# Kernel tuning notes

Hardware: AMD Instinct MI355X
Metric: run time of the kernel (lower is better)

The kernel has to match this reference:

```python
import jax, jax.numpy as jnp
import numpy as np

D_MODEL = 1024
NUM_HEADS = 16
ROPE_THETA = 10000.0


def setup_inputs() -> dict:
    key = jax.random.key(0)
    ks = jax.random.split(key, 5)
    B, S, D = 4, 2048, D_MODEL
    std = (2.0 / (D * D)) ** 0.5
    return {
        "x": jax.random.normal(ks[0], (B, S, D), dtype=jnp.float32),
        "Wq": jax.random.normal(ks[1], (D, D), dtype=jnp.float32) * std,
        "Wk": jax.random.normal(ks[2], (D, D), dtype=jnp.float32) * std,
        "Wv": jax.random.normal(ks[3], (D, D), dtype=jnp.float32) * std,
        "Wo": jax.random.normal(ks[4], (D, D), dtype=jnp.float32) * std,
    }


def _apply_rope(t, sin, cos):
    # t: [B, H, S, d_k]; sin/cos: [S, d_k//2] (broadcast over B, H)
    e = t[..., 0::2]
    o = t[..., 1::2]
    rot = jnp.stack((e * cos - o * sin, e * sin + o * cos), axis=-1)
    return rot.reshape(t.shape)  # interleave back to d_k


def reference(x, Wq, Wk, Wv, Wo):
    B, S, D = x.shape
    H = NUM_HEADS
    dk = D // H

    def proj(W):
        y = jnp.einsum('bsd,ed->bse', x, W)  # Linear: weight is [out, in]
        return y.reshape(B, S, H, dk).transpose(0, 2, 1, 3)  # [B,H,S,dk]

    q, k, v = proj(Wq), proj(Wk), proj(Wv)

    # RoPE cache (token_positions = arange(S))
    half = dk // 2
    inv_freq = 1.0 / (ROPE_THETA ** (jnp.arange(half, dtype=jnp.float32) * 2.0 / dk))
    angles = jnp.arange(S, dtype=jnp.float32)[:, None] * inv_freq[None, :]  # [S, half]
    sin, cos = jnp.sin(angles), jnp.cos(angles)
    q = _apply_rope(q, sin, cos)
    k = _apply_rope(k, sin, cos)

    # scaled dot-product attention with causal mask
    scores = jnp.einsum('bhqd,bhkd->bhqk', q, k) / jnp.sqrt(jnp.float32(dk))
    causal = jnp.tril(jnp.ones((S, S), dtype=bool))
    scores = jnp.where(causal, scores, jnp.finfo(scores.dtype).min)
    p = jax.nn.softmax(scores, axis=-1)
    out = jnp.einsum('bhqk,bhkd->bhqd', p, v)  # [B,H,S,dk]

    out = out.transpose(0, 2, 1, 3).reshape(B, S, D)
    return jnp.einsum('bsd,ed->bse', out, Wo)
```

## Files before the change

kernel.cpp:

```cpp
#include <hip/hip_runtime.h>

typedef unsigned short u16;
typedef unsigned int   u32;

typedef short    short8 __attribute__((ext_vector_type(8)));
typedef __bf16   bf16x8 __attribute__((ext_vector_type(8)));
typedef _Float16 half8  __attribute__((ext_vector_type(8)));
typedef float    f32x4  __attribute__((ext_vector_type(4)));

#define S_LEN   2048
#define DM      1024
#define NHEAD   16
#define DK      64
#define BH_TOT  64
#define M_TOK   8192
#define KDIM    1024

__device__ __forceinline__ u16 f2bf(float f) {
    u32 u = __builtin_bit_cast(u32, f);
    u += 0x7FFFu + ((u >> 16) & 1u);
    return (u16)(u >> 16);
}
__device__ __forceinline__ float bf2f(u16 h) {
    u32 u = ((u32)h) << 16;
    return __builtin_bit_cast(float, u);
}
__device__ __forceinline__ f32x4 mfma_bf16(short8 a, short8 b, f32x4 c) {
    return __builtin_amdgcn_mfma_f32_16x16x32_bf16(
        __builtin_bit_cast(bf16x8, a), __builtin_bit_cast(bf16x8, b), c, 0, 0, 0);
}
__device__ __forceinline__ f32x4 mfma_f16(half8 a, half8 b, f32x4 c) {
    return __builtin_amdgcn_mfma_f32_16x16x32_f16(a, b, c, 0, 0, 0);
}
__device__ __forceinline__ u32 pk_f16(float a, float b) {
    return __builtin_bit_cast(u32, __builtin_amdgcn_cvt_pkrtz(a, b));
}
__device__ __forceinline__ void gl_lds16(const void* g, void* l) {
    __builtin_amdgcn_global_load_lds(
        (const __attribute__((address_space(1))) u32*)g,
        (__attribute__((address_space(3))) u32*)l, 16, 0, 0);
}
__device__ __forceinline__ void bar_raw() { asm volatile("s_barrier" ::: "memory"); }
__device__ __forceinline__ void wait_vm4() { asm volatile("s_waitcnt vmcnt(4)" ::: "memory"); }
__device__ __forceinline__ void wait_vm0() { asm volatile("s_waitcnt vmcnt(0)" ::: "memory"); }

__device__ __forceinline__ int perm_inv(int rc) {
    const int nt = rc >> 4, mid = (rc >> 2) & 3, r = rc & 3;
    return 32 * (nt >> 1) + 8 * mid + 4 * (nt & 1) + r;
}

__global__ void cvt_bf16_v4(const float4* __restrict__ in, uint2* __restrict__ out, int n4) {
    int i = blockIdx.x * 256 + threadIdx.x;
    if (i >= n4) return;
    float4 f = in[i];
    uint2 o;
    o.x = (u32)f2bf(f.x) | ((u32)f2bf(f.y) << 16);
    o.y = (u32)f2bf(f.z) | ((u32)f2bf(f.w) << 16);
    out[i] = o;
}

__global__ void rope_qk(u16* __restrict__ Qb, u16* __restrict__ Kb) {
    int idx = blockIdx.x * 256 + threadIdx.x;
    const int PER = BH_TOT * S_LEN * 32;
    u16* T = (idx < PER) ? Qb : Kb;
    int i2 = (idx < PER) ? idx : idx - PER;
    int i  = i2 & 31;
    int s  = (i2 >> 5) & 2047;
    int bh = i2 >> 16;
    u32* p = (u32*)T + (size_t)(bh * S_LEN + s) * 32 + i;
    u32 v = *p;
    float e = bf2f((u16)(v & 0xFFFF));
    float o = bf2f((u16)(v >> 16));
    float inv = expf(-(float)i * 0.287823136624255f);
    float ang = (float)s * inv;
    float sn = sinf(ang), cs = cosf(ang);
    float e2 = e * cs - o * sn;
    float o2 = e * sn + o * cs;
    *p = (u32)f2bf(e2) | ((u32)f2bf(o2) << 16);
}

template <int MODE>
__global__ __launch_bounds__(256)
void gemm_nt(const u16* __restrict__ A, const u16* __restrict__ Bw,
             u16* __restrict__ oQ, u16* __restrict__ oK, u16* __restrict__ oVt,
             float* __restrict__ oF) {
    __shared__ u16 As[128 * 32];
    __shared__ u16 Bs[128 * 32];
    const int tid  = threadIdx.x;
    const int wave = tid >> 6, lane = tid & 63;
    const int quad = lane >> 4, l15 = lane & 15;
    const int wr = wave >> 1, wc = wave & 1;
    const int mbase = blockIdx.y * 128;
    const int nbase = blockIdx.x * 128;

    f32x4 acc[4][4];
#pragma unroll
    for (int i = 0; i < 4; i++)
#pragma unroll
        for (int j = 0; j < 4; j++) acc[i][j] = (f32x4)0.0f;

    const int c0 = wave * 2, c1 = wave * 2 + 1;
    const int srow0 = c0 * 16 + (lane >> 2);
    const int srow1 = c1 * 16 + (lane >> 2);
    const int scolb = (lane & 3) * 16;

    for (int kk = 0; kk < KDIM; kk += 32) {
        gl_lds16((const char*)(A  + (size_t)(mbase + srow0) * KDIM + kk) + scolb,
                 (char*)As + c0 * 1024 + lane * 16);
        gl_lds16((const char*)(A  + (size_t)(mbase + srow1) * KDIM + kk) + scolb,
                 (char*)As + c1 * 1024 + lane * 16);
        gl_lds16((const char*)(Bw + (size_t)(nbase + srow0) * KDIM + kk) + scolb,
                 (char*)Bs + c0 * 1024 + lane * 16);
        gl_lds16((const char*)(Bw + (size_t)(nbase + srow1) * KDIM + kk) + scolb,
                 (char*)Bs + c1 * 1024 + lane * 16);
        __syncthreads();

        short8 af[4], bf[4];
#pragma unroll
        for (int mt = 0; mt < 4; mt++)
            af[mt] = *(const short8*)&As[(wr * 64 + mt * 16 + l15) * 32 + quad * 8];
#pragma unroll
        for (int nt = 0; nt < 4; nt++)
            bf[nt] = *(const short8*)&Bs[(wc * 64 + nt * 16 + l15) * 32 + quad * 8];
#pragma unroll
        for (int mt = 0; mt < 4; mt++)
#pragma unroll
            for (int nt = 0; nt < 4; nt++)
                acc[mt][nt] = mfma_bf16(af[mt], bf[nt], acc[mt][nt]);
        __syncthreads();
    }

#pragma unroll
    for (int mt = 0; mt < 4; mt++) {
#pragma unroll
        for (int nt = 0; nt < 4; nt++) {
            const int n  = nbase + wc * 64 + nt * 16 + l15;
            const int mb = mbase + wr * 64 + mt * 16 + quad * 4;
            f32x4 v = acc[mt][nt];
            if (MODE == 0) {
                const int proj = n >> 10;
                const int e = n & 1023;
                const int h = e >> 6, d = e & 63;
                if (proj == 2) {
                    const int b = mb >> 11, s = mb & 2047;
                    const int bh = b * NHEAD + h;
                    uint2 pk;
                    pk.x = pk_f16(v[0], v[1]);
                    pk.y = pk_f16(v[2], v[3]);
                    *(uint2*)&oVt[((size_t)bh * DK + d) * S_LEN + s] = pk;
                } else {
                    u16* dst = (proj == 0) ? oQ : oK;
#pragma unroll
                    for (int r = 0; r < 4; r++) {
                        const int m = mb + r;
                        const int b = m >> 11, s = m & 2047;
                        const int bh = b * NHEAD + h;
                        dst[((size_t)bh * S_LEN + s) * DK + d] = f2bf(v[r]);
                    }
                }
            } else {
#pragma unroll
                for (int r = 0; r < 4; r++)
                    oF[(size_t)(mb + r) * DM + n] = v[r];
            }
        }
    }
}

__global__ __launch_bounds__(256)
void flash_attn(const u16* __restrict__ Q, const u16* __restrict__ K,
                const u16* __restrict__ Vt, u16* __restrict__ Oc) {
    __shared__ u16 Ks[2][64 * 64];
    __shared__ u16 Vs[2][64 * 64];
    const int qt = 31 - (int)blockIdx.y;
    const int bh = blockIdx.x;
    const int tid  = threadIdx.x;
    const int wave = tid >> 6, lane = tid & 63;
    const int quad = lane >> 4, l15 = lane & 15;
    const int x7 = l15 & 7;
    const size_t headQK = (size_t)bh * S_LEN * DK;
    const size_t headVt = (size_t)bh * DK * S_LEN;
    const int b = bh >> 4, h = bh & 15;
    const float SCL = 0.18033688011112042f;

    half8 ones;
#pragma unroll
    for (int j = 0; j < 8; j++) ones[j] = (_Float16)1.0f;

    const int rwl  = lane >> 3;
    const int scol = (lane & 7) ^ rwl;
    const int rc0 = wave * 16 + rwl, rc1 = rc0 + 8;
    const u16* gK0 = K  + headQK + (size_t)perm_inv(rc0) * DK + scol * 8;
    const u16* gK1 = K  + headQK + (size_t)perm_inv(rc1) * DK + scol * 8;
    const u16* gV0 = Vt + headVt + (size_t)rc0 * S_LEN + scol * 8;
    const u16* gV1 = Vt + headVt + (size_t)rc1 * S_LEN + scol * 8;
    const int ldsOff = wave * 2048 + lane * 16;
    const int koff0 = (quad ^ x7) * 8;
    const int koff1 = ((4 + quad) ^ x7) * 8;

    const int qrow = qt * 64 + wave * 16 + l15;
    const short8 qf0 = *(const short8*)&Q[headQK + (size_t)qrow * DK + quad * 8];
    const short8 qf1 = *(const short8*)&Q[headQK + (size_t)qrow * DK + 32 + quad * 8];

    float m_st = -__builtin_inff();
    f32x4 lacc = (f32x4)0.0f;
    f32x4 oacc[4];
#pragma unroll
    for (int n = 0; n < 4; n++) oacc[n] = (f32x4)0.0f;

    gl_lds16(gK0, (char*)Ks[0] + ldsOff);
    gl_lds16(gK1, (char*)Ks[0] + ldsOff + 1024);
    gl_lds16(gV0, (char*)Vs[0] + ldsOff);
    gl_lds16(gV1, (char*)Vs[0] + ldsOff + 1024);

    for (int kt = 0; kt <= qt; kt++) {
        const int cur = kt & 1, nxt = cur ^ 1;
        bar_raw();
        {
            const int ktn = (kt < qt) ? kt + 1 : qt;
            gl_lds16(gK0 + (size_t)ktn * 64 * DK, (char*)Ks[nxt] + ldsOff);
            gl_lds16(gK1 + (size_t)ktn * 64 * DK, (char*)Ks[nxt] + ldsOff + 1024);
            gl_lds16(gV0 + ktn * 64,              (char*)Vs[nxt] + ldsOff);
            gl_lds16(gV1 + ktn * 64,              (char*)Vs[nxt] + ldsOff + 1024);
        }
        wait_vm4();
        bar_raw();

        f32x4 sc[4];
#pragma unroll
        for (int nt = 0; nt < 4; nt++) {
            const int rb = (nt * 16 + l15) * 64;
            short8 kf0 = *(const short8*)&Ks[cur][rb + koff0];
            short8 kf1 = *(const short8*)&Ks[cur][rb + koff1];
            f32x4 z = (f32x4)0.0f;
            z = mfma_bf16(kf0, qf0, z);
            z = mfma_bf16(kf1, qf1, z);
#pragma unroll
            for (int r = 0; r < 4; r++) z[r] *= SCL;
            sc[nt] = z;
        }
        if (kt == qt) {
            const int qloc = wave * 16 + l15;
#pragma unroll
            for (int nt = 0; nt < 4; nt++) {
                const int kb = 32 * (nt >> 1) + 8 * quad + 4 * (nt & 1);
#pragma unroll
                for (int r = 0; r < 4; r++)
                    if (kb + r > qloc) sc[nt][r] = -__builtin_inff();
            }
        }
        float mx0 = fmaxf(fmaxf(sc[0][0], sc[0][1]), fmaxf(sc[0][2], sc[0][3]));
        float mx1 = fmaxf(fmaxf(sc[1][0], sc[1][1]), fmaxf(sc[1][2], sc[1][3]));
        float mx2 = fmaxf(fmaxf(sc[2][0], sc[2][1]), fmaxf(sc[2][2], sc[2][3]));
        float mx3 = fmaxf(fmaxf(sc[3][0], sc[3][1]), fmaxf(sc[3][2], sc[3][3]));
        float mx = fmaxf(fmaxf(mx0, mx1), fmaxf(mx2, mx3));
        mx = fmaxf(mx, __shfl_xor(mx, 16));
        mx = fmaxf(mx, __shfl_xor(mx, 32));
        const float mn = fmaxf(m_st, mx);
        const float alpha = __builtin_amdgcn_exp2f(m_st - mn);
        m_st = mn;
#pragma unroll
        for (int nt = 0; nt < 4; nt++)
#pragma unroll
            for (int r = 0; r < 4; r++)
                sc[nt][r] = __builtin_amdgcn_exp2f(sc[nt][r] - m_st);
        u32 pw[8];
        pw[0] = pk_f16(sc[0][0], sc[0][1]); pw[1] = pk_f16(sc[0][2], sc[0][3]);
        pw[2] = pk_f16(sc[1][0], sc[1][1]); pw[3] = pk_f16(sc[1][2], sc[1][3]);
        pw[4] = pk_f16(sc[2][0], sc[2][1]); pw[5] = pk_f16(sc[2][2], sc[2][3]);
        pw[6] = pk_f16(sc[3][0], sc[3][1]); pw[7] = pk_f16(sc[3][2], sc[3][3]);
        half8 pf0 = __builtin_bit_cast(half8, *(uint4*)&pw[0]);
        half8 pf1 = __builtin_bit_cast(half8, *(uint4*)&pw[4]);
        float alr[4];
#pragma unroll
        for (int r = 0; r < 4; r++) alr[r] = __shfl(alpha, quad * 20 + r);
#pragma unroll
        for (int n = 0; n < 4; n++)
#pragma unroll
            for (int r = 0; r < 4; r++) oacc[n][r] *= alr[r];
#pragma unroll
        for (int r = 0; r < 4; r++) lacc[r] *= alr[r];
#pragma unroll
        for (int c = 0; c < 2; c++) {
            const half8 pf = c ? pf1 : pf0;
            lacc = mfma_f16(pf, ones, lacc);
            const int voff = ((c * 4 + quad) ^ x7) * 8;
#pragma unroll
            for (int nt2 = 0; nt2 < 4; nt2++) {
                half8 vf = __builtin_bit_cast(half8,
                    *(const short8*)&Vs[cur][(nt2 * 16 + l15) * 64 + voff]);
                oacc[nt2] = mfma_f16(pf, vf, oacc[nt2]);
            }
        }
    }
    wait_vm0();

#pragma unroll
    for (int r = 0; r < 4; r++) {
        const float inv = 1.0f / lacc[r];
        const int s = qt * 64 + wave * 16 + quad * 4 + r;
#pragma unroll
        for (int nt2 = 0; nt2 < 4; nt2++)
            Oc[((size_t)(b * S_LEN + s)) * DM + h * 64 + nt2 * 16 + l15] =
                f2bf(oacc[nt2][r] * inv);
    }
}

#define OFF_XBF  ((size_t)0)
#define OFF_WCAT ((size_t)8388608)
#define OFF_WO   ((size_t)11534336)
#define OFF_QB   ((size_t)12582912)
#define OFF_KB   ((size_t)20971520)
#define OFF_VT   ((size_t)29360128)

extern "C" void kernel_launch(void* const* d_in, const int* in_sizes, int n_in,
                              void* d_out, int out_size, void* d_ws, size_t ws_size,
                              hipStream_t stream) {
    const float* x  = (const float*)d_in[0];
    const float* Wq = (const float*)d_in[1];
    const float* Wk = (const float*)d_in[2];
    const float* Wv = (const float*)d_in[3];
    const float* Wo = (const float*)d_in[4];
    u16* ws  = (u16*)d_ws;
    u16* XBF = ws + OFF_XBF;
    u16* WCA = ws + OFF_WCAT;
    u16* WOB = ws + OFF_WO;
    u16* QB  = ws + OFF_QB;
    u16* KB  = ws + OFF_KB;
    u16* VT  = ws + OFF_VT;
    u16* AT  = XBF;

    cvt_bf16_v4<<<8192, 256, 0, stream>>>((const float4*)x,  (uint2*)XBF, 2097152);
    cvt_bf16_v4<<<1024, 256, 0, stream>>>((const float4*)Wq, (uint2*)(WCA),            262144);
    cvt_bf16_v4<<<1024, 256, 0, stream>>>((const float4*)Wk, (uint2*)(WCA + 1048576),  262144);
    cvt_bf16_v4<<<1024, 256, 0, stream>>>((const float4*)Wv, (uint2*)(WCA + 2097152),  262144);
    cvt_bf16_v4<<<1024, 256, 0, stream>>>((const float4*)Wo, (uint2*)WOB, 262144);

    gemm_nt<0><<<dim3(24, 64), 256, 0, stream>>>(XBF, WCA, QB, KB, VT, nullptr);
    rope_qk<<<32768, 256, 0, stream>>>(QB, KB);
    flash_attn<<<dim3(64, 32), 256, 0, stream>>>(QB, KB, VT, AT);
    gemm_nt<1><<<dim3(8, 64), 256, 0, stream>>>(AT, WOB, nullptr, nullptr, nullptr,
                                                (float*)d_out);
}
```

Baseline: 291.3 us.

## Double-buffer GEMM LDS tiles with async prefetch and XOR swizzle

Converts the projection GEMM main loop to double-buffered LDS so the next K-tile's direct global-to-LDS loads are issued before computing on the current tile, with explicit vmcnt waits and raw barriers. It also XOR-swizzles the 16-byte column chunks in LDS to cut bank conflicts on the MFMA fragment reads. The aim is to hide global load latency behind the MFMAs, at the cost of double the shared memory per block, which may lower occupancy. The last iteration issues a redundant reload of the same tile.

New measurement: 296.3 us. Within noise of the previous version (+1.7%).

```diff
diff --git a/kernel.cpp b/kernel.cpp
--- a/kernel.cpp
+++ b/kernel.cpp
@@ -84,8 +84,8 @@
 void gemm_nt(const u16* __restrict__ A, const u16* __restrict__ Bw,
              u16* __restrict__ oQ, u16* __restrict__ oK, u16* __restrict__ oVt,
              float* __restrict__ oF) {
-    __shared__ u16 As[128 * 32];
-    __shared__ u16 Bs[128 * 32];
+    __shared__ u16 As[2][128 * 32];
+    __shared__ u16 Bs[2][128 * 32];
     const int tid  = threadIdx.x;
     const int wave = tid >> 6, lane = tid & 63;
     const int quad = lane >> 4, l15 = lane & 15;
@@ -99,36 +99,49 @@
 #pragma unroll
         for (int j = 0; j < 4; j++) acc[i][j] = (f32x4)0.0f;
 
-    const int c0 = wave * 2, c1 = wave * 2 + 1;
-    const int srow0 = c0 * 16 + (lane >> 2);
-    const int srow1 = c1 * 16 + (lane >> 2);
-    const int scolb = (lane & 3) * 16;
-
-    for (int kk = 0; kk < KDIM; kk += 32) {
-        gl_lds16((const char*)(A  + (size_t)(mbase + srow0) * KDIM + kk) + scolb,
-                 (char*)As + c0 * 1024 + lane * 16);
-        gl_lds16((const char*)(A  + (size_t)(mbase + srow1) * KDIM + kk) + scolb,
-                 (char*)As + c1 * 1024 + lane * 16);
-        gl_lds16((const char*)(Bw + (size_t)(nbase + srow0) * KDIM + kk) + scolb,
-                 (char*)Bs + c0 * 1024 + lane * 16);
-        gl_lds16((const char*)(Bw + (size_t)(nbase + srow1) * KDIM + kk) + scolb,
-                 (char*)Bs + c1 * 1024 + lane * 16);
-        __syncthreads();
+    const int srow0 = wave * 32 + (lane >> 2);
+    const int srow1 = srow0 + 16;
+    const int scolb = ((lane & 3) ^ ((lane >> 3) & 3)) * 16;
+    const int ldsOff = wave * 2048 + lane * 16;
+    const u16* gA0 = A  + (size_t)(mbase + srow0) * KDIM;
+    const u16* gA1 = A  + (size_t)(mbase + srow1) * KDIM;
+    const u16* gB0 = Bw + (size_t)(nbase + srow0) * KDIM;
+    const u16* gB1 = Bw + (size_t)(nbase + srow1) * KDIM;
+    const int koffq = (quad ^ ((l15 >> 1) & 3)) * 8;
+
+    gl_lds16((const char*)gA0 + scolb, (char*)As[0] + ldsOff);
+    gl_lds16((const char*)gA1 + scolb, (char*)As[0] + ldsOff + 1024);
+    gl_lds16((const char*)gB0 + scolb, (char*)Bs[0] + ldsOff);
+    gl_lds16((const char*)gB1 + scolb, (char*)Bs[0] + ldsOff + 1024);
+
+    const int KT = KDIM / 32;
+    for (int kt = 0; kt < KT; kt++) {
+        const int cur = kt & 1, nxt = cur ^ 1;
+        bar_raw();
+        {
+            const int kkn = (kt + 1 < KT) ? (kt + 1) * 32 : kt * 32;
+            gl_lds16((const char*)(gA0 + kkn) + scolb, (char*)As[nxt] + ldsOff);
+            gl_lds16((const char*)(gA1 + kkn) + scolb, (char*)As[nxt] + ldsOff + 1024);
+            gl_lds16((const char*)(gB0 + kkn) + scolb, (char*)Bs[nxt] + ldsOff);
+            gl_lds16((const char*)(gB1 + kkn) + scolb, (char*)Bs[nxt] + ldsOff + 1024);
+        }
+        wait_vm4();
+        bar_raw();
 
         short8 af[4], bf[4];
 #pragma unroll
         for (int mt = 0; mt < 4; mt++)
-            af[mt] = *(const short8*)&As[(wr * 64 + mt * 16 + l15) * 32 + quad * 8];
+            af[mt] = *(const short8*)&As[cur][(wr * 64 + mt * 16 + l15) * 32 + koffq];
 #pragma unroll
         for (int nt = 0; nt < 4; nt++)
-            bf[nt] = *(const short8*)&Bs[(wc * 64 + nt * 16 + l15) * 32 + quad * 8];
+            bf[nt] = *(const short8*)&Bs[cur][(wc * 64 + nt * 16 + l15) * 32 + koffq];
 #pragma unroll
         for (int mt = 0; mt < 4; mt++)
 #pragma unroll
             for (int nt = 0; nt < 4; nt++)
                 acc[mt][nt] = mfma_bf16(af[mt], bf[nt], acc[mt][nt]);
-        __syncthreads();
     }
+    wait_vm0();
 
 #pragma unroll
     for (int mt = 0; mt < 4; mt++) {
```

## Replace LDS-staged GEMM with direct global-to-register loads and double buffering

Applied to the files above, without the earlier changes.

The projection and output GEMMs no longer stage A and B tiles through shared memory with barriers. Each wave now loads its MFMA fragments straight from global memory into registers, double-buffered across K steps. This removes LDS traffic and __syncthreads, but each fragment is loaded separately by the two waves that share it, which doubles global/L2 traffic. The per-lane loads are also only 16 bytes wide, which may coalesce poorly.

Measured after the change: 424.2 us. 1.46x slower.

```diff
diff --git a/kernel.cpp b/kernel.cpp
--- a/kernel.cpp
+++ b/kernel.cpp
@@ -81,11 +81,9 @@
 
 template <int MODE>
 __global__ __launch_bounds__(256)
-void gemm_nt(const u16* __restrict__ A, const u16* __restrict__ Bw,
-             u16* __restrict__ oQ, u16* __restrict__ oK, u16* __restrict__ oVt,
-             float* __restrict__ oF) {
-    __shared__ u16 As[128 * 32];
-    __shared__ u16 Bs[128 * 32];
+void gemm_reg(const u16* __restrict__ A, const u16* __restrict__ Bw,
+              u16* __restrict__ oQ, u16* __restrict__ oK, u16* __restrict__ oVt,
+              float* __restrict__ oF) {
     const int tid  = threadIdx.x;
     const int wave = tid >> 6, lane = tid & 63;
     const int quad = lane >> 4, l15 = lane & 15;
@@ -93,41 +91,42 @@
     const int mbase = blockIdx.y * 128;
     const int nbase = blockIdx.x * 128;
 
+    const char* pA[4];
+    const char* pB[4];
+#pragma unroll
+    for (int i = 0; i < 4; i++) {
+        pA[i] = (const char*)(A  + (size_t)(mbase + wr * 64 + i * 16 + l15) * KDIM + quad * 8);
+        pB[i] = (const char*)(Bw + (size_t)(nbase + wc * 64 + i * 16 + l15) * KDIM + quad * 8);
+    }
+
     f32x4 acc[4][4];
 #pragma unroll
     for (int i = 0; i < 4; i++)
 #pragma unroll
         for (int j = 0; j < 4; j++) acc[i][j] = (f32x4)0.0f;
 
-    const int c0 = wave * 2, c1 = wave * 2 + 1;
-    const int srow0 = c0 * 16 + (lane >> 2);
-    const int srow1 = c1 * 16 + (lane >> 2);
-    const int scolb = (lane & 3) * 16;
-
-    for (int kk = 0; kk < KDIM; kk += 32) {
-        gl_lds16((const char*)(A  + (size_t)(mbase + srow0) * KDIM + kk) + scolb,
-                 (char*)As + c0 * 1024 + lane * 16);
-        gl_lds16((const char*)(A  + (size_t)(mbase + srow1) * KDIM + kk) + scolb,
-                 (char*)As + c1 * 1024 + lane * 16);
-        gl_lds16((const char*)(Bw + (size_t)(nbase + srow0) * KDIM + kk) + scolb,
-                 (char*)Bs + c0 * 1024 + lane * 16);
-        gl_lds16((const char*)(Bw + (size_t)(nbase + srow1) * KDIM + kk) + scolb,
-                 (char*)Bs + c1 * 1024 + lane * 16);
-        __syncthreads();
-
-        short8 af[4], bf[4];
+    short8 a[2][4], b[2][4];
+#pragma unroll
+    for (int i = 0; i < 4; i++) {
+        a[0][i] = *(const short8*)pA[i];
+        b[0][i] = *(const short8*)pB[i];
+    }
+#pragma unroll
+    for (int kt = 0; kt < 32; kt++) {
+        const int cur = kt & 1, nxt = cur ^ 1;
+        if (kt < 31) {
+            const int off = (kt + 1) * 64;
+#pragma unroll
+            for (int i = 0; i < 4; i++) {
+                a[nxt][i] = *(const short8*)(pA[i] + off);
+                b[nxt][i] = *(const short8*)(pB[i] + off);
+            }
+        }
 #pragma unroll
         for (int mt = 0; mt < 4; mt++)
-            af[mt] = *(const short8*)&As[(wr * 64 + mt * 16 + l15) * 32 + quad * 8];
-#pragma unroll
-        for (int nt = 0; nt < 4; nt++)
-            bf[nt] = *(const short8*)&Bs[(wc * 64 + nt * 16 + l15) * 32 + quad * 8];
-#pragma unroll
-        for (int mt = 0; mt < 4; mt++)
 #pragma unroll
             for (int nt = 0; nt < 4; nt++)
-                acc[mt][nt] = mfma_bf16(af[mt], bf[nt], acc[mt][nt]);
-        __syncthreads();
+                acc[mt][nt] = mfma_bf16(a[cur][mt], b[cur][nt], acc[mt][nt]);
     }
 
 #pragma unroll
@@ -142,8 +141,8 @@
                 const int e = n & 1023;
                 const int h = e >> 6, d = e & 63;
                 if (proj == 2) {
-                    const int b = mb >> 11, s = mb & 2047;
-                    const int bh = b * NHEAD + h;
+                    const int b_ = mb >> 11, s = mb & 2047;
+                    const int bh = b_ * NHEAD + h;
                     uint2 pk;
                     pk.x = pk_f16(v[0], v[1]);
                     pk.y = pk_f16(v[2], v[3]);
@@ -153,8 +152,8 @@
 #pragma unroll
                     for (int r = 0; r < 4; r++) {
                         const int m = mb + r;
-                        const int b = m >> 11, s = m & 2047;
-                        const int bh = b * NHEAD + h;
+                        const int b_ = m >> 11, s = m & 2047;
+                        const int bh = b_ * NHEAD + h;
                         dst[((size_t)bh * S_LEN + s) * DK + d] = f2bf(v[r]);
                     }
                 }
@@ -336,9 +335,9 @@
     cvt_bf16_v4<<<1024, 256, 0, stream>>>((const float4*)Wv, (uint2*)(WCA + 2097152),  262144);
     cvt_bf16_v4<<<1024, 256, 0, stream>>>((const float4*)Wo, (uint2*)WOB, 262144);
 
-    gemm_nt<0><<<dim3(24, 64), 256, 0, stream>>>(XBF, WCA, QB, KB, VT, nullptr);
+    gemm_reg<0><<<dim3(24, 64), 256, 0, stream>>>(XBF, WCA, QB, KB, VT, nullptr);
     rope_qk<<<32768, 256, 0, stream>>>(QB, KB);
     flash_attn<<<dim3(64, 32), 256, 0, stream>>>(QB, KB, VT, AT);
-    gemm_nt<1><<<dim3(8, 64), 256, 0, stream>>>(AT, WOB, nullptr, nullptr, nullptr,
-                                                (float*)d_out);
-}
+    gemm_reg<1><<<dim3(8, 64), 256, 0, stream>>>(AT, WOB, nullptr, nullptr, nullptr,
+                                                 (float*)d_out);
+}
```
